# Kernel tuning notes

Hardware: AMD Instinct MI355X
Metric: run time of the kernel (lower is better)

The kernel has to match this reference:

```python
import jax, jax.numpy as jnp
import numpy as np

SCALE = 10.0
TEMP = 0.5
SIM_TH = 0.7
EPOCH = 1
KL_WEIGHT = max(0.5 * (1 - EPOCH / 60), 0.1)
NEG_INF = -1e30


def _normalize(x, eps=1e-12):
    n = jnp.linalg.norm(x, axis=-1, keepdims=True)
    return x / jnp.maximum(n, eps)


def setup_inputs() -> dict:
    key = jax.random.key(0)
    ks = jax.random.split(key, 6)
    P, B, D, N, K = 4, 128, 512, 32768, 10
    # 0.02 scale keeps pairwise distances O(1) so exp(-SCALE*dist) does not underflow
    feature = jax.random.normal(ks[0], (P, B, D), jnp.float32) * 0.02
    text_feature = jax.random.normal(ks[1], (B, P, D), jnp.float32) * 0.02
    centers = jax.random.normal(ks[2], (P, N, D), jnp.float32) * 0.02
    position = jax.random.randint(ks[3], (B,), 0, N)
    cross_indices = jax.random.randint(ks[4], (B, K), 0, N)
    vid = jax.random.randint(ks[5], (N,), 0, 751)
    return {"feature": feature, "text_feature": text_feature, "centers": centers,
            "position": position, "cross_indices": cross_indices, "vid": vid}


def _align_loss(feature, text_feature):
    # feature: [P,B,D]; text_feature: [B,P,D] (detached in original)
    img = _normalize(feature)
    txt = _normalize(jax.lax.stop_gradient(jnp.transpose(text_feature, (1, 0, 2))))
    img_sim = jnp.einsum('pbd,pcd->pbc', img, img) / TEMP   # [P,B,B]
    txt_sim = jnp.einsum('pbd,pcd->pbc', txt, txt) / TEMP
    mask = (img_sim > SIM_TH) & (txt_sim > SIM_TH)
    valid = mask.any(-1)                                   # [P,B] row/col validity
    colm = valid[:, None, :]                               # mask over columns
    il = jnp.where(colm, img_sim, NEG_INF)
    tl = jnp.where(colm, txt_sim, NEG_INF)
    img_logp = jax.nn.log_softmax(il, -1)
    txt_logp = jax.nn.log_softmax(tl, -1)                  # fully detached (txt detached)
    txt_prob = jnp.exp(txt_logp)
    img_logp_sg = jax.lax.stop_gradient(img_logp)
    img_prob = jnp.exp(img_logp_sg)
    # F.kl_div(input=log q, target=p) = sum p*(log p - log q), batchmean over valid rows
    kl1 = jnp.sum(jnp.where(colm, txt_prob * (txt_logp - img_logp), 0.0), -1)      # [P,B]
    kl2 = jnp.sum(jnp.where(colm, img_prob * (img_logp_sg - txt_logp), 0.0), -1)
    nvalid = valid.sum(-1)                                 # [P]
    r1 = jnp.sum(jnp.where(valid, kl1, 0.0), -1)
    r2 = jnp.sum(jnp.where(valid, kl2, 0.0), -1)
    per_part = 0.5 * (r1 + r2) / jnp.maximum(nvalid, 1)
    return jnp.sum(jnp.where(nvalid > 0, per_part, 0.0))


def _contrastive_loss(feature, centers, position, cross_indices):
    P, B, D = feature.shape
    N = centers.shape[1]
    pos_feats = jnp.take(centers, cross_indices, axis=1)   # [P,B,K,D]
    fn2 = jnp.sum(feature * feature, -1)                   # [P,B]
    pn2 = jnp.sum(pos_feats * pos_feats, -1)               # [P,B,K]
    pd2 = fn2[..., None] + pn2 - 2.0 * jnp.einsum('pbd,pbkd->pbk', feature, pos_feats)
    pos_dist = jnp.sqrt(jnp.maximum(pd2, 1e-12))           # [P,B,K]
    cn2 = jnp.sum(centers * centers, -1)                   # [P,N]
    nd2 = fn2[..., None] + cn2[:, None, :] - 2.0 * jnp.einsum('pbd,pnd->pbn', feature, centers)
    neg_dist = jnp.sqrt(jnp.maximum(nd2, 1e-12))           # [P,B,N]
    neg_mask = (jnp.ones((N,), bool)
                .at[cross_indices.reshape(-1)].set(False)
                .at[position].set(False))
    x = jnp.log(jnp.sum(jnp.exp(-SCALE * pos_dist), -1))   # [P,B]
    ey = jnp.exp(-SCALE * neg_dist) * neg_mask[None, None, :].astype(neg_dist.dtype)
    y = jnp.log(jnp.sum(ey, -1))                           # [P,B]
    l = jnp.sum(y - x, -1) / B                             # per-part, div by feature.size(1)
    l = jnp.where(jnp.isnan(l), 0.0, l)
    return jnp.sum(l) / P


def reference(feature, text_feature, centers, position, cross_indices, vid):
    align_loss = _align_loss(feature, text_feature)
    contrastive_loss = _contrastive_loss(feature, centers, position, cross_indices)
    total_loss = contrastive_loss + KL_WEIGHT * align_loss
    pos_vid = jnp.take(vid, cross_indices, axis=0)         # [B,K]
    return total_loss, contrastive_loss, align_loss, pos_vid
```

## Files before the change

kernel.cpp:

```cpp
#include <hip/hip_runtime.h>
#include <hip/hip_bf16.h>
#include <math.h>

#define P_ 4
#define B_ 128
#define D_ 512
#define N_ 32768
#define K_ 10
#define TNB 128
#define NT2 (N_ / TNB)
#define BKC 64
#define KP 72

typedef __attribute__((ext_vector_type(8))) short bf16x8;
typedef __attribute__((ext_vector_type(4))) float f32x4;

static __device__ __forceinline__ float block_sum_128(float v, float* sh) {
    const int t = threadIdx.x;
    sh[t] = v; __syncthreads();
    #pragma unroll
    for (int s = 64; s > 0; s >>= 1) { if (t < s) sh[t] += sh[t + s]; __syncthreads(); }
    float r = sh[0]; __syncthreads();
    return r;
}
static __device__ __forceinline__ float block_max_128(float v, float* sh) {
    const int t = threadIdx.x;
    sh[t] = v; __syncthreads();
    #pragma unroll
    for (int s = 64; s > 0; s >>= 1) { if (t < s) sh[t] = fmaxf(sh[t], sh[t + s]); __syncthreads(); }
    float r = sh[0]; __syncthreads();
    return r;
}

static __device__ __forceinline__ uint2 pack_bf16x4(float4 v) {
    union { __hip_bfloat162 h; unsigned u; } lo, hi;
    lo.h = __float22bfloat162_rn(make_float2(v.x, v.y));
    hi.h = __float22bfloat162_rn(make_float2(v.z, v.w));
    uint2 r; r.x = lo.u; r.y = hi.u;
    return r;
}

__global__ void mask_init_kernel(float* __restrict__ m) {
    int i = blockIdx.x * 256 + threadIdx.x;
    if (i < N_) m[i] = 1.0f;
}
__global__ void mask_zero_kernel(const int* __restrict__ cross,
                                 const int* __restrict__ pos,
                                 float* __restrict__ m) {
    int i = blockIdx.x * 256 + threadIdx.x;
    if (i < B_ * K_) m[cross[i]] = 0.0f;
    else if (i < B_ * K_ + B_) m[pos[i - B_ * K_]] = 0.0f;
}

__global__ void norm_kernel(const float* __restrict__ feature,
                            const float* __restrict__ text_feature,
                            float* __restrict__ img, float* __restrict__ txt,
                            float* __restrict__ fn2) {
    const int pb = blockIdx.x;
    const int p = pb >> 7, b = pb & 127;
    const int which = blockIdx.y;
    const int t = threadIdx.x;
    const float* src = (which == 0) ? feature + (size_t)pb * D_
                                    : text_feature + ((size_t)b * P_ + p) * D_;
    float v0 = src[t], v1 = src[t + 256];
    __shared__ float sred[256];
    sred[t] = v0 * v0 + v1 * v1;
    __syncthreads();
    #pragma unroll
    for (int s = 128; s > 0; s >>= 1) { if (t < s) sred[t] += sred[t + s]; __syncthreads(); }
    const float ss = sred[0];
    const float inv = 1.0f / fmaxf(sqrtf(ss), 1e-12f);
    float* dst = (which == 0) ? img : txt;
    dst[(size_t)pb * D_ + t] = v0 * inv;
    dst[(size_t)pb * D_ + t + 256] = v1 * inv;
    if (which == 0 && t == 0) fn2[pb] = ss;
}

__global__ void sim_kernel(const float* __restrict__ img,
                           const float* __restrict__ txt,
                           float* __restrict__ img_sim,
                           float* __restrict__ txt_sim,
                           float* __restrict__ validf) {
    const int p = blockIdx.x;
    const int b0 = blockIdx.y * 2;
    const int c = threadIdx.x;
    __shared__ float ai[2][D_];
    __shared__ float at[2][D_];
    __shared__ int flags[2];
    #pragma unroll
    for (int i = 0; i < 8; ++i) {
        int idx = c + i * 128;
        int row = idx >> 9, d = idx & 511;
        ai[row][d] = img[(size_t)(p * B_ + b0 + row) * D_ + d];
        at[row][d] = txt[(size_t)(p * B_ + b0 + row) * D_ + d];
    }
    if (c < 2) flags[c] = 0;
    __syncthreads();
    float di[2] = {0, 0};
    float dt[2] = {0, 0};
    const float* ic = img + (size_t)(p * B_ + c) * D_;
    const float* tc = txt + (size_t)(p * B_ + c) * D_;
    for (int d = 0; d < D_; d += 4) {
        float4 vi = *(const float4*)(ic + d);
        float4 vt = *(const float4*)(tc + d);
        #pragma unroll
        for (int i = 0; i < 2; ++i) {
            di[i] += ai[i][d] * vi.x + ai[i][d + 1] * vi.y + ai[i][d + 2] * vi.z + ai[i][d + 3] * vi.w;
            dt[i] += at[i][d] * vt.x + at[i][d + 1] * vt.y + at[i][d + 2] * vt.z + at[i][d + 3] * vt.w;
        }
    }
    #pragma unroll
    for (int i = 0; i < 2; ++i) {
        float is = 2.0f * di[i];
        float ts = 2.0f * dt[i];
        img_sim[(size_t)(p * B_ + b0 + i) * B_ + c] = is;
        txt_sim[(size_t)(p * B_ + b0 + i) * B_ + c] = ts;
        if (is > 0.7f && ts > 0.7f) flags[i] = 1;
    }
    __syncthreads();
    if (c < 2) validf[p * B_ + b0 + c] = (float)flags[c];
}

__global__ void kl_kernel(const float* __restrict__ img_sim,
                          const float* __restrict__ txt_sim,
                          const float* __restrict__ validf,
                          float* __restrict__ klrow) {
    const int p = blockIdx.x, r = blockIdx.y;
    const int c = threadIdx.x;
    __shared__ float sh[128];
    const size_t base = (size_t)(p * B_ + r) * B_;
    const bool val = validf[p * B_ + c] > 0.5f;
    const float il = val ? img_sim[base + c] : -1e30f;
    const float tl = val ? txt_sim[base + c] : -1e30f;
    const float mi = block_max_128(il, sh);
    const float mt = block_max_128(tl, sh);
    const float si = block_sum_128(expf(il - mi), sh);
    const float st = block_sum_128(expf(tl - mt), sh);
    const float lsei = mi + logf(si);
    const float lset = mt + logf(st);
    float term = 0.0f;
    if (val) {
        float lpi = il - lsei;
        float lpt = tl - lset;
        term = expf(lpt) * (lpt - lpi) + expf(lpi) * (lpi - lpt);
    }
    const float ks = block_sum_128(term, sh);
    if (c == 0) klrow[p * B_ + r] = (validf[p * B_ + r] > 0.5f) ? ks : 0.0f;
}

__global__ void posx_kernel(const float* __restrict__ feature,
                            const float* __restrict__ centers,
                            const float* __restrict__ fn2,
                            const int* __restrict__ cross,
                            float* __restrict__ xarr) {
    const int pb = blockIdx.x;
    const int p = pb >> 7, b = pb & 127;
    const int l = threadIdx.x;
    const float* f = feature + (size_t)pb * D_;
    float4 f0 = *(const float4*)(f + l * 4);
    float4 f1 = *(const float4*)(f + 256 + l * 4);
    const float fn2v = fn2[pb];
    float ex = 0.0f;
    #pragma unroll
    for (int k = 0; k < K_; ++k) {
        int idx = cross[b * K_ + k];
        const float* cp = centers + ((size_t)p * N_ + idx) * D_;
        float4 c0 = *(const float4*)(cp + l * 4);
        float4 c1 = *(const float4*)(cp + 256 + l * 4);
        float dot = f0.x * c0.x + f0.y * c0.y + f0.z * c0.z + f0.w * c0.w
                  + f1.x * c1.x + f1.y * c1.y + f1.z * c1.z + f1.w * c1.w;
        float pn2 = c0.x * c0.x + c0.y * c0.y + c0.z * c0.z + c0.w * c0.w
                  + c1.x * c1.x + c1.y * c1.y + c1.z * c1.z + c1.w * c1.w;
        #pragma unroll
        for (int off = 32; off > 0; off >>= 1) {
            dot += __shfl_down(dot, off);
            pn2 += __shfl_down(pn2, off);
        }
        if (l == 0) {
            float d2 = fn2v + pn2 - 2.0f * dot;
            ex += expf(-10.0f * sqrtf(fmaxf(d2, 1e-12f)));
        }
    }
    if (l == 0) xarr[pb] = logf(ex);
}

__global__ __launch_bounds__(256) void neg_mfma_kernel(
    const float* __restrict__ feature,
    const float* __restrict__ centers,
    const float* __restrict__ fn2,
    const float* __restrict__ maskf,
    float* __restrict__ Spart) {
    const int tile = blockIdx.x;
    const int p = blockIdx.y;
    const int n0g = tile * TNB;
    const int t = threadIdx.x;
    const int l = t & 63;
    const int w = t >> 6;
    const int m0w = (w & 1) * 64;
    const int n0w = (w >> 1) * 64;

    __shared__ unsigned short As[128 * KP];
    __shared__ unsigned short Bs[128 * KP];
    __shared__ float cn2s[128];
    __shared__ float red[128];
    __shared__ float fn2s[128];

    if (t < 128) { red[t] = 0.0f; fn2s[t] = fn2[p * B_ + t]; }

    f32x4 acc[4][4];
    #pragma unroll
    for (int i = 0; i < 4; ++i)
        #pragma unroll
        for (int j = 0; j < 4; ++j) acc[i][j] = (f32x4)0.0f;

    float c2acc[8];
    #pragma unroll
    for (int i = 0; i < 8; ++i) c2acc[i] = 0.0f;

    const float* Ab = feature + (size_t)p * B_ * D_;
    const float* Bb = centers + ((size_t)p * N_ + n0g) * D_;

    const int lrow = t >> 4;
    const int c4 = t & 15;

    for (int kk = 0; kk < D_; kk += BKC) {
        float4 va[8], vb[8];
        #pragma unroll
        for (int i = 0; i < 8; ++i) {
            const int row = lrow + i * 16;
            va[i] = *(const float4*)(Ab + (size_t)row * D_ + kk + c4 * 4);
            vb[i] = *(const float4*)(Bb + (size_t)row * D_ + kk + c4 * 4);
        }
        __syncthreads();
        #pragma unroll
        for (int i = 0; i < 8; ++i) {
            const int row = lrow + i * 16;
            *(uint2*)&As[row * KP + c4 * 4] = pack_bf16x4(va[i]);
            *(uint2*)&Bs[row * KP + c4 * 4] = pack_bf16x4(vb[i]);
            float s = vb[i].x * vb[i].x + vb[i].y * vb[i].y
                    + vb[i].z * vb[i].z + vb[i].w * vb[i].w;
            s += __shfl_xor(s, 1); s += __shfl_xor(s, 2);
            s += __shfl_xor(s, 4); s += __shfl_xor(s, 8);
            c2acc[i] += s;
        }
        __syncthreads();
        #pragma unroll
        for (int ks = 0; ks < 2; ++ks) {
            bf16x8 af[4], bf[4];
            const int ko = ks * 32 + (l >> 4) * 8;
            #pragma unroll
            for (int i = 0; i < 4; ++i) {
                af[i] = *(const bf16x8*)&As[(m0w + i * 16 + (l & 15)) * KP + ko];
                bf[i] = *(const bf16x8*)&Bs[(n0w + i * 16 + (l & 15)) * KP + ko];
            }
            #pragma unroll
            for (int i = 0; i < 4; ++i)
                #pragma unroll
                for (int j = 0; j < 4; ++j)
                    acc[i][j] = __builtin_amdgcn_mfma_f32_16x16x32_bf16(
                        af[i], bf[j], acc[i][j], 0, 0, 0);
        }
    }
    if (c4 == 0) {
        #pragma unroll
        for (int i = 0; i < 8; ++i) cn2s[lrow + i * 16] = c2acc[i];
    }
    __syncthreads();

    float c2l[4], mkl[4];
    #pragma unroll
    for (int j = 0; j < 4; ++j) {
        const int col = n0w + j * 16 + (l & 15);
        c2l[j] = cn2s[col];
        mkl[j] = maskf[n0g + col];
    }
    #pragma unroll
    for (int i = 0; i < 4; ++i) {
        #pragma unroll
        for (int r = 0; r < 4; ++r) {
            const int row = m0w + i * 16 + (l >> 4) * 4 + r;
            const float fv = fn2s[row];
            float s = 0.0f;
            #pragma unroll
            for (int j = 0; j < 4; ++j) {
                const float nd2 = fv + c2l[j] - 2.0f * acc[i][j][r];
                s += mkl[j] * __expf(-10.0f * sqrtf(fmaxf(nd2, 1e-12f)));
            }
            s += __shfl_xor(s, 1); s += __shfl_xor(s, 2);
            s += __shfl_xor(s, 4); s += __shfl_xor(s, 8);
            if ((l & 15) == 0) atomicAdd(&red[row], s);
        }
    }
    __syncthreads();
    if (t < 128) Spart[(size_t)(p * B_ + t) * NT2 + tile] = red[t];
}

__global__ void red_kernel(const float* __restrict__ Spart,
                           const float* __restrict__ xarr,
                           float* __restrict__ diff) {
    const int pb = blockIdx.x;
    const int t = threadIdx.x;
    __shared__ float sh[128];
    const float* sp = Spart + (size_t)pb * NT2;
    float s = sp[t] + sp[t + 128];
    float S = block_sum_128(s, sh);
    if (t == 0) diff[pb] = logf(S) - xarr[pb];
}

__global__ void final_kernel(const float* __restrict__ validf,
                             const float* __restrict__ klrow,
                             const float* __restrict__ diff,
                             float* __restrict__ out) {
    const int t = threadIdx.x;
    __shared__ float sh[128];
    __shared__ float accum[2];
    if (t == 0) { accum[0] = 0.0f; accum[1] = 0.0f; }
    __syncthreads();
    for (int p = 0; p < P_; ++p) {
        float nv = block_sum_128(validf[p * B_ + t], sh);
        float ks = block_sum_128(klrow[p * B_ + t], sh);
        float ds = block_sum_128(diff[p * B_ + t], sh);
        if (t == 0) {
            float lp = ds / (float)B_;
            if (!(lp != lp)) accum[0] += lp;
            if (nv > 0.5f) accum[1] += 0.5f * ks / fmaxf(nv, 1.0f);
        }
        __syncthreads();
    }
    if (t == 0) {
        float contrastive = accum[0] / (float)P_;
        float align = accum[1];
        out[1] = contrastive;
        out[2] = align;
        out[0] = contrastive + 0.49166666666666664f * align;
    }
}

__global__ void posvid_kernel(const int* __restrict__ cross,
                              const int* __restrict__ vid,
                              float* __restrict__ out) {
    int i = blockIdx.x * 256 + threadIdx.x;
    if (i < B_ * K_) out[3 + i] = (float)vid[cross[i]];
}

extern "C" void kernel_launch(void* const* d_in, const int* in_sizes, int n_in,
                              void* d_out, int out_size, void* d_ws, size_t ws_size,
                              hipStream_t stream) {
    const float* feature      = (const float*)d_in[0];
    const float* text_feature = (const float*)d_in[1];
    const float* centers      = (const float*)d_in[2];
    const int*   position     = (const int*)d_in[3];
    const int*   cross        = (const int*)d_in[4];
    const int*   vid          = (const int*)d_in[5];
    float* out = (float*)d_out;

    float* ws      = (float*)d_ws;
    float* img     = ws;
    float* txt     = img + (size_t)P_ * B_ * D_;
    float* fn2     = txt + (size_t)P_ * B_ * D_;
    float* img_sim = fn2 + P_ * B_;
    float* txt_sim = img_sim + P_ * B_ * B_;
    float* validf  = txt_sim + P_ * B_ * B_;
    float* klrow   = validf + P_ * B_;
    float* xarr    = klrow + P_ * B_;
    float* maskf   = xarr + P_ * B_;
    float* diff    = maskf + N_;
    float* Spart   = diff + P_ * B_;

    mask_init_kernel<<<N_ / 256, 256, 0, stream>>>(maskf);
    mask_zero_kernel<<<(B_ * K_ + B_ + 255) / 256, 256, 0, stream>>>(cross, position, maskf);
    norm_kernel<<<dim3(P_ * B_, 2), 256, 0, stream>>>(feature, text_feature, img, txt, fn2);
    sim_kernel<<<dim3(P_, B_ / 2), 128, 0, stream>>>(img, txt, img_sim, txt_sim, validf);
    kl_kernel<<<dim3(P_, B_), 128, 0, stream>>>(img_sim, txt_sim, validf, klrow);
    posx_kernel<<<P_ * B_, 64, 0, stream>>>(feature, centers, fn2, cross, xarr);
    neg_mfma_kernel<<<dim3(NT2, P_), 256, 0, stream>>>(feature, centers, fn2, maskf, Spart);
    red_kernel<<<P_ * B_, 128, 0, stream>>>(Spart, xarr, diff);
    final_kernel<<<1, 128, 0, stream>>>(validf, klrow, diff, out);
    posvid_kernel<<<(B_ * K_ + 255) / 256, 256, 0, stream>>>(cross, vid, out);
}
```

Before: 451.2 us.

## Prefetch centers into double-buffered LDS, pre-convert feature to bf16, warp-level KL

The neg_mfma kernel now double-buffers the centers tile in LDS, loading the next K-chunk from global memory while MFMAs run on the current one. This halves the per-iteration barriers. The feature matrix is converted to bf16 once in a new prep kernel, and MFMA A-fragments are read straight from global or cache instead of being staged through LDS. The center-norm shuffle reduction moves out of the loop, and the KL kernel now uses one wavefront per row with shuffle reductions instead of shared-memory block reductions. The trade-off is more repeated global reads of A fragments per block, plus an extra kernel pass over feature.

```diff
diff --git a/kernel.cpp b/kernel.cpp
--- a/kernel.cpp
+++ b/kernel.cpp
@@ -23,14 +23,6 @@
     float r = sh[0]; __syncthreads();
     return r;
 }
-static __device__ __forceinline__ float block_max_128(float v, float* sh) {
-    const int t = threadIdx.x;
-    sh[t] = v; __syncthreads();
-    #pragma unroll
-    for (int s = 64; s > 0; s >>= 1) { if (t < s) sh[t] = fmaxf(sh[t], sh[t + s]); __syncthreads(); }
-    float r = sh[0]; __syncthreads();
-    return r;
-}
 
 static __device__ __forceinline__ uint2 pack_bf16x4(float4 v) {
     union { __hip_bfloat162 h; unsigned u; } lo, hi;
@@ -40,10 +32,15 @@
     return r;
 }
 
-__global__ void mask_init_kernel(float* __restrict__ m) {
+__global__ void prep_kernel(const float* __restrict__ feature,
+                            unsigned short* __restrict__ featbf,
+                            float* __restrict__ maskf) {
     int i = blockIdx.x * 256 + threadIdx.x;
-    if (i < N_) m[i] = 1.0f;
-}
+    float4 v = ((const float4*)feature)[i];
+    ((uint2*)featbf)[i] = pack_bf16x4(v);
+    if (i < N_) maskf[i] = 1.0f;
+}
+
 __global__ void mask_zero_kernel(const int* __restrict__ cross,
                                  const int* __restrict__ pos,
                                  float* __restrict__ m) {
@@ -121,31 +118,49 @@
     if (c < 2) validf[p * B_ + b0 + c] = (float)flags[c];
 }
 
-__global__ void kl_kernel(const float* __restrict__ img_sim,
-                          const float* __restrict__ txt_sim,
-                          const float* __restrict__ validf,
-                          float* __restrict__ klrow) {
-    const int p = blockIdx.x, r = blockIdx.y;
-    const int c = threadIdx.x;
-    __shared__ float sh[128];
+__global__ __launch_bounds__(256) void kl_kernel(
+    const float* __restrict__ img_sim,
+    const float* __restrict__ txt_sim,
+    const float* __restrict__ validf,
+    float* __restrict__ klrow) {
+    const int l = threadIdx.x & 63;
+    const int wv = threadIdx.x >> 6;
+    const int p = blockIdx.x;
+    const int r = blockIdx.y * 4 + wv;
     const size_t base = (size_t)(p * B_ + r) * B_;
-    const bool val = validf[p * B_ + c] > 0.5f;
-    const float il = val ? img_sim[base + c] : -1e30f;
-    const float tl = val ? txt_sim[base + c] : -1e30f;
-    const float mi = block_max_128(il, sh);
-    const float mt = block_max_128(tl, sh);
-    const float si = block_sum_128(expf(il - mi), sh);
-    const float st = block_sum_128(expf(tl - mt), sh);
+    const bool v0 = validf[p * B_ + l] > 0.5f;
+    const bool v1 = validf[p * B_ + 64 + l] > 0.5f;
+    const float il0 = v0 ? img_sim[base + l] : -1e30f;
+    const float il1 = v1 ? img_sim[base + 64 + l] : -1e30f;
+    const float tl0 = v0 ? txt_sim[base + l] : -1e30f;
+    const float tl1 = v1 ? txt_sim[base + 64 + l] : -1e30f;
+    float mi = fmaxf(il0, il1), mt = fmaxf(tl0, tl1);
+    #pragma unroll
+    for (int off = 32; off > 0; off >>= 1) {
+        mi = fmaxf(mi, __shfl_xor(mi, off));
+        mt = fmaxf(mt, __shfl_xor(mt, off));
+    }
+    float si = expf(il0 - mi) + expf(il1 - mi);
+    float st = expf(tl0 - mt) + expf(tl1 - mt);
+    #pragma unroll
+    for (int off = 32; off > 0; off >>= 1) {
+        si += __shfl_xor(si, off);
+        st += __shfl_xor(st, off);
+    }
     const float lsei = mi + logf(si);
     const float lset = mt + logf(st);
     float term = 0.0f;
-    if (val) {
-        float lpi = il - lsei;
-        float lpt = tl - lset;
-        term = expf(lpt) * (lpt - lpi) + expf(lpi) * (lpi - lpt);
-    }
-    const float ks = block_sum_128(term, sh);
-    if (c == 0) klrow[p * B_ + r] = (validf[p * B_ + r] > 0.5f) ? ks : 0.0f;
+    if (v0) {
+        float lpi = il0 - lsei, lpt = tl0 - lset;
+        term += expf(lpt) * (lpt - lpi) + expf(lpi) * (lpi - lpt);
+    }
+    if (v1) {
+        float lpi = il1 - lsei, lpt = tl1 - lset;
+        term += expf(lpt) * (lpt - lpi) + expf(lpi) * (lpi - lpt);
+    }
+    #pragma unroll
+    for (int off = 32; off > 0; off >>= 1) term += __shfl_xor(term, off);
+    if (l == 0) klrow[p * B_ + r] = (validf[p * B_ + r] > 0.5f) ? term : 0.0f;
 }
 
 __global__ void posx_kernel(const float* __restrict__ feature,
@@ -185,7 +200,7 @@
 }
 
 __global__ __launch_bounds__(256) void neg_mfma_kernel(
-    const float* __restrict__ feature,
+    const unsigned short* __restrict__ featbf,
     const float* __restrict__ centers,
     const float* __restrict__ fn2,
     const float* __restrict__ maskf,
@@ -199,8 +214,7 @@
     const int m0w = (w & 1) * 64;
     const int n0w = (w >> 1) * 64;
 
-    __shared__ unsigned short As[128 * KP];
-    __shared__ unsigned short Bs[128 * KP];
+    __shared__ unsigned short Bs[2][128 * KP];
     __shared__ float cn2s[128];
     __shared__ float red[128];
     __shared__ float fn2s[128];
@@ -217,53 +231,68 @@
     #pragma unroll
     for (int i = 0; i < 8; ++i) c2acc[i] = 0.0f;
 
-    const float* Ab = feature + (size_t)p * B_ * D_;
+    const unsigned short* Ab = featbf + (size_t)p * B_ * D_;
     const float* Bb = centers + ((size_t)p * N_ + n0g) * D_;
 
     const int lrow = t >> 4;
     const int c4 = t & 15;
 
+    float4 vb[8];
+    #pragma unroll
+    for (int i = 0; i < 8; ++i)
+        vb[i] = *(const float4*)(Bb + (size_t)(lrow + i * 16) * D_ + c4 * 4);
+    #pragma unroll
+    for (int i = 0; i < 8; ++i) {
+        const int row = lrow + i * 16;
+        *(uint2*)&Bs[0][row * KP + c4 * 4] = pack_bf16x4(vb[i]);
+        c2acc[i] += vb[i].x * vb[i].x + vb[i].y * vb[i].y
+                  + vb[i].z * vb[i].z + vb[i].w * vb[i].w;
+    }
+    __syncthreads();
+
     for (int kk = 0; kk < D_; kk += BKC) {
-        float4 va[8], vb[8];
-        #pragma unroll
-        for (int i = 0; i < 8; ++i) {
-            const int row = lrow + i * 16;
-            va[i] = *(const float4*)(Ab + (size_t)row * D_ + kk + c4 * 4);
-            vb[i] = *(const float4*)(Bb + (size_t)row * D_ + kk + c4 * 4);
-        }
-        __syncthreads();
-        #pragma unroll
-        for (int i = 0; i < 8; ++i) {
-            const int row = lrow + i * 16;
-            *(uint2*)&As[row * KP + c4 * 4] = pack_bf16x4(va[i]);
-            *(uint2*)&Bs[row * KP + c4 * 4] = pack_bf16x4(vb[i]);
-            float s = vb[i].x * vb[i].x + vb[i].y * vb[i].y
-                    + vb[i].z * vb[i].z + vb[i].w * vb[i].w;
-            s += __shfl_xor(s, 1); s += __shfl_xor(s, 2);
-            s += __shfl_xor(s, 4); s += __shfl_xor(s, 8);
-            c2acc[i] += s;
-        }
-        __syncthreads();
+        const int cur = (kk >> 6) & 1;
+        const int nxt = cur ^ 1;
+        const bool more = (kk + BKC) < D_;
+        if (more) {
+            #pragma unroll
+            for (int i = 0; i < 8; ++i)
+                vb[i] = *(const float4*)(Bb + (size_t)(lrow + i * 16) * D_ + (kk + BKC) + c4 * 4);
+        }
         #pragma unroll
         for (int ks = 0; ks < 2; ++ks) {
-            bf16x8 af[4], bf[4];
+            bf16x8 af[4], bfr[4];
             const int ko = ks * 32 + (l >> 4) * 8;
             #pragma unroll
             for (int i = 0; i < 4; ++i) {
-                af[i] = *(const bf16x8*)&As[(m0w + i * 16 + (l & 15)) * KP + ko];
-                bf[i] = *(const bf16x8*)&Bs[(n0w + i * 16 + (l & 15)) * KP + ko];
+                af[i]  = *(const bf16x8*)(Ab + (size_t)(m0w + i * 16 + (l & 15)) * D_ + kk + ko);
+                bfr[i] = *(const bf16x8*)&Bs[cur][(n0w + i * 16 + (l & 15)) * KP + ko];
             }
             #pragma unroll
             for (int i = 0; i < 4; ++i)
                 #pragma unroll
                 for (int j = 0; j < 4; ++j)
                     acc[i][j] = __builtin_amdgcn_mfma_f32_16x16x32_bf16(
-                        af[i], bf[j], acc[i][j], 0, 0, 0);
-        }
-    }
-    if (c4 == 0) {
-        #pragma unroll
-        for (int i = 0; i < 8; ++i) cn2s[lrow + i * 16] = c2acc[i];
+                        af[i], bfr[j], acc[i][j], 0, 0, 0);
+        }
+        if (more) {
+            #pragma unroll
+            for (int i = 0; i < 8; ++i) {
+                const int row = lrow + i * 16;
+                *(uint2*)&Bs[nxt][row * KP + c4 * 4] = pack_bf16x4(vb[i]);
+                c2acc[i] += vb[i].x * vb[i].x + vb[i].y * vb[i].y
+                          + vb[i].z * vb[i].z + vb[i].w * vb[i].w;
+            }
+        }
+        __syncthreads();
+    }
+
+    #pragma unroll
+    for (int i = 0; i < 8; ++i) {
+        float s = c2acc[i];
+        s += __shfl_xor(s, 1); s += __shfl_xor(s, 2);
+        s += __shfl_xor(s, 4); s += __shfl_xor(s, 8);
+        if (c4 == 0) cn2s[lrow + i * 16] = s;
     }
     __syncthreads();
 
@@ -366,14 +395,15 @@
     float* maskf   = xarr + P_ * B_;
     float* diff    = maskf + N_;
     float* Spart   = diff + P_ * B_;
-
-    mask_init_kernel<<<N_ / 256, 256, 0, stream>>>(maskf);
+    unsigned short* featbf = (unsigned short*)(Spart + (size_t)P_ * B_ * NT2);
+
+    prep_kernel<<<P_ * B_ * D_ / 4 / 256, 256, 0, stream>>>(feature, featbf, maskf);
     mask_zero_kernel<<<(B_ * K_ + B_ + 255) / 256, 256, 0, stream>>>(cross, position, maskf);
     norm_kernel<<<dim3(P_ * B_, 2), 256, 0, stream>>>(feature, text_feature, img, txt, fn2);
     sim_kernel<<<dim3(P_, B_ / 2), 128, 0, stream>>>(img, txt, img_sim, txt_sim, validf);
-    kl_kernel<<<dim3(P_, B_), 128, 0, stream>>>(img_sim, txt_sim, validf, klrow);
+    kl_kernel<<<dim3(P_, B_ / 4), 256, 0, stream>>>(img_sim, txt_sim, validf, klrow);
     posx_kernel<<<P_ * B_, 64, 0, stream>>>(feature, centers, fn2, cross, xarr);
-    neg_mfma_kernel<<<dim3(NT2, P_), 256, 0, stream>>>(feature, centers, fn2, maskf, Spart);
+    neg_mfma_kernel<<<dim3(NT2, P_), 256, 0, stream>>>(featbf, centers, fn2, maskf, Spart);
     red_kernel<<<P_ * B_, 128, 0, stream>>>(Spart, xarr, diff);
     final_kernel<<<1, 128, 0, stream>>>(validf, klrow, diff, out);
     posvid_kernel<<<(B_ * K_ + 255) / 256, 256, 0, stream>>>(cross, vid, out);
```

After: 457.6 us. Within noise of the previous version (+1.4%).
